# Kernel tuning notes

Hardware: AMD Instinct MI355X
Metric: run time of the kernel (lower is better)

## Reference

```python
import jax, jax.numpy as jnp
import numpy as np

NUM_CODEBOOKS = 32
CODEBOOK_SIZE = 1024
CODE_DIM = 64
BATCH = 4096
INIT_SCALE = 0.1


def setup_inputs() -> dict:
    key = jax.random.key(0)
    k1, k2 = jax.random.split(key)
    z = jax.random.normal(k1, (BATCH, NUM_CODEBOOKS * CODE_DIM), dtype=jnp.float32)
    codebook = jax.random.uniform(
        k2, (NUM_CODEBOOKS, CODEBOOK_SIZE, CODE_DIM),
        minval=-INIT_SCALE, maxval=INIT_SCALE, dtype=jnp.float32)
    return {"z": z, "codebook": codebook}


def reference(z, codebook):
    B = z.shape[0]
    G, K, D = codebook.shape
    z_groups = z.reshape(B, G, D)                                   # [B,G,D]
    # squared euclidean distances: ||z||^2 - 2 z.c + ||c||^2 -> [B,G,K]
    z2 = jnp.sum(z_groups * z_groups, axis=-1, keepdims=True)       # [B,G,1]
    c2 = jnp.sum(codebook * codebook, axis=-1)                      # [G,K]
    zc = jnp.einsum('bgd,gkd->bgk', z_groups, codebook)             # [B,G,K]
    distances = z2 - 2.0 * zc + c2[None, :, :]
    indices = jnp.argmin(distances, axis=-1)                        # [B,G] int
    # gather codebook[g, indices[b,g]] -> [B,G,D]
    z_q_groups = codebook[jnp.arange(G)[None, :], indices]
    commitment_loss = jnp.mean((z_groups - jax.lax.stop_gradient(z_q_groups)) ** 2)
    codebook_loss = jnp.mean((z_q_groups - jax.lax.stop_gradient(z_groups)) ** 2)
    z_st_groups = z_groups + jax.lax.stop_gradient(z_q_groups - z_groups)
    # usage histogram over codebook entries, averaged over (B,G)
    counts = jnp.zeros((K,), dtype=jnp.float32).at[indices.reshape(-1)].add(1.0)
    usage = counts / jnp.float32(B * G)
    entropy = -jnp.sum(usage * jnp.log(usage + 1e-10))
    perplexity = jnp.exp(entropy)
    quantized_flat = z_st_groups.reshape(B, G * D)
    return (quantized_flat, indices, commitment_loss, codebook_loss, entropy, perplexity)
```

## Files before the change

kernel.cpp:

```cpp
#include <hip/hip_runtime.h>
#include <math.h>

#define NG 32
#define NK 1024
#define ND 64
#define NB 4096
#define KSPLIT 4
#define KCHUNK (NK / KSPLIT)


__global__ void vq_init(int* __restrict__ counts, float* __restrict__ losssum) {
    int i = blockIdx.x * blockDim.x + threadIdx.x;
    if (i < NK) counts[i] = 0;
    if (i == 0) *losssum = 0.f;
}

__global__ void vq_c2(const float* __restrict__ cb, float* __restrict__ c2) {
    int i = blockIdx.x * blockDim.x + threadIdx.x;
    if (i >= NG * NK) return;
    const float* c = cb + (size_t)i * ND;
    float s0 = 0.f, s1 = 0.f, s2 = 0.f, s3 = 0.f;
#pragma unroll
    for (int d = 0; d < ND; d += 4) {
        float4 v = *reinterpret_cast<const float4*>(c + d);
        s0 = fmaf(v.x, v.x, s0);
        s1 = fmaf(v.y, v.y, s1);
        s2 = fmaf(v.z, v.z, s2);
        s3 = fmaf(v.w, v.w, s3);
    }
    c2[i] = (s0 + s1) + (s2 + s3);
}

template <int W>
__device__ __forceinline__ float epi_slice(const float* __restrict__ cbest,
                                           float* __restrict__ qrow,
                                           const float (&zv)[ND]) {
    float l0 = 0.f, l1 = 0.f, l2 = 0.f, l3 = 0.f;
#pragma unroll
    for (int i = 0; i < 4; i++) {
        float4 c = reinterpret_cast<const float4*>(cbest)[W * 4 + i];
        float zx = zv[W * 16 + 4 * i + 0], zy = zv[W * 16 + 4 * i + 1];
        float zz = zv[W * 16 + 4 * i + 2], zw = zv[W * 16 + 4 * i + 3];
        float4 st;
        st.x = zx + (c.x - zx);
        st.y = zy + (c.y - zy);
        st.z = zz + (c.z - zz);
        st.w = zw + (c.w - zw);
        reinterpret_cast<float4*>(qrow)[W * 4 + i] = st;
        float dx = zx - c.x, dy = zy - c.y, dz = zz - c.z, dw = zw - c.w;
        l0 = fmaf(dx, dx, l0); l1 = fmaf(dy, dy, l1);
        l2 = fmaf(dz, dz, l2); l3 = fmaf(dw, dw, l3);
    }
    return (l0 + l1) + (l2 + l3);
}

__global__ __launch_bounds__(256) void vq_main(
        const float* __restrict__ z, const float* __restrict__ cb,
        const float* __restrict__ c2, float* __restrict__ qout,
        float* __restrict__ idxout, int* __restrict__ counts,
        float* __restrict__ losssum) {
    const int tid = threadIdx.x;
    const int lane = tid & 63;
    const int wu = __builtin_amdgcn_readfirstlane(tid >> 6);
    const int g = blockIdx.x & (NG - 1);
    const int rowblk = blockIdx.x >> 5;
    const int row = rowblk * 64 + lane;

    const float* zrow = z + (size_t)row * (NG * ND) + (size_t)g * ND;
    float zv[ND];
#pragma unroll
    for (int i = 0; i < ND / 4; i++) {
        float4 v = reinterpret_cast<const float4*>(zrow)[i];
        zv[4 * i + 0] = v.x; zv[4 * i + 1] = v.y;
        zv[4 * i + 2] = v.z; zv[4 * i + 3] = v.w;
    }
    float t0 = 0.f, t1 = 0.f, t2 = 0.f, t3 = 0.f;
#pragma unroll
    for (int d = 0; d < ND; d += 4) {
        t0 = fmaf(zv[d + 0], zv[d + 0], t0);
        t1 = fmaf(zv[d + 1], zv[d + 1], t1);
        t2 = fmaf(zv[d + 2], zv[d + 2], t2);
        t3 = fmaf(zv[d + 3], zv[d + 3], t3);
    }
    const float z2 = (t0 + t1) + (t2 + t3);

    const float* cg = cb + (size_t)g * NK * ND;
    const float* c2g = c2 + (size_t)g * NK;
    const int k0 = wu * KCHUNK;

    float best = 3.402823466e38f;
    int bestk = k0;
#pragma unroll 1
    for (int k = k0; k < k0 + KCHUNK; k++) {
        const float* ck = cg + (size_t)k * ND;
        float a0 = 0.f, a1 = 0.f, a2 = 0.f, a3 = 0.f;
#pragma unroll
        for (int d = 0; d < ND; d += 4) {
            a0 = fmaf(zv[d + 0], ck[d + 0], a0);
            a1 = fmaf(zv[d + 1], ck[d + 1], a1);
            a2 = fmaf(zv[d + 2], ck[d + 2], a2);
            a3 = fmaf(zv[d + 3], ck[d + 3], a3);
        }
        float zc = (a0 + a1) + (a2 + a3);
        float dist = (z2 - 2.0f * zc) + c2g[k];
        if (dist < best) { best = dist; bestk = k; }
    }

    __shared__ float s_best[KSPLIT][64];
    __shared__ int s_bk[KSPLIT][64];
    __shared__ int s_win[64];
    s_best[wu][lane] = best;
    s_bk[wu][lane] = bestk;
    __syncthreads();
    if (wu == 0) {
        float b = s_best[0][lane];
        int bk = s_bk[0][lane];
#pragma unroll
        for (int q = 1; q < KSPLIT; q++) {
            float d = s_best[q][lane];
            int kk = s_bk[q][lane];
            if (d < b) { b = d; bk = kk; }
        }
        s_win[lane] = bk;
        idxout[(size_t)row * NG + g] = (float)bk;
        atomicAdd(&counts[bk], 1);
    }
    __syncthreads();

    const int bk = s_win[lane];
    const float* cbest = cg + (size_t)bk * ND;
    float* qrow = qout + (size_t)row * (NG * ND) + (size_t)g * ND;
    float lsum;
    switch (wu) {
        case 0: lsum = epi_slice<0>(cbest, qrow, zv); break;
        case 1: lsum = epi_slice<1>(cbest, qrow, zv); break;
        case 2: lsum = epi_slice<2>(cbest, qrow, zv); break;
        default: lsum = epi_slice<3>(cbest, qrow, zv); break;
    }
#pragma unroll
    for (int off = 32; off > 0; off >>= 1) lsum += __shfl_down(lsum, off, 64);
    if (lane == 0) atomicAdd(losssum, lsum);
}

__global__ void vq_final(const int* __restrict__ counts,
                         const float* __restrict__ losssum,
                         float* __restrict__ out) {
    __shared__ float red[256];
    int tid = threadIdx.x;
    float e = 0.f;
    for (int k = tid; k < NK; k += 256) {
        float u = (float)counts[k] * (1.0f / 131072.0f);
        e -= u * logf(u + 1e-10f);
    }
    red[tid] = e;
    __syncthreads();
    for (int s = 128; s > 0; s >>= 1) {
        if (tid < s) red[tid] += red[tid + s];
        __syncthreads();
    }
    if (tid == 0) {
        float loss = *losssum * (1.0f / 8388608.0f);
        float ent = red[0];
        out[0] = loss;
        out[1] = loss;
        out[2] = ent;
        out[3] = expf(ent);
    }
}

extern "C" void kernel_launch(void* const* d_in, const int* in_sizes, int n_in,
                              void* d_out, int out_size, void* d_ws, size_t ws_size,
                              hipStream_t stream) {
    const float* z = (const float*)d_in[0];
    const float* cb = (const float*)d_in[1];
    float* out = (float*)d_out;
    float* qout = out;
    float* idxout = out + (size_t)NB * NG * ND;
    float* scal = idxout + (size_t)NB * NG;

    float* c2 = (float*)d_ws;
    int* counts = (int*)(c2 + NG * NK);
    float* losssum = (float*)(counts + NK);

    vq_init<<<(NK + 255) / 256, 256, 0, stream>>>(counts, losssum);
    vq_c2<<<(NG * NK + 255) / 256, 256, 0, stream>>>(cb, c2);
    vq_main<<<(NB / 64) * NG, 256, 0, stream>>>(z, cb, c2, qout, idxout, counts, losssum);
    vq_final<<<1, 256, 0, stream>>>(counts, losssum, scal);
}
```

Before: 502.5 us.

## Software-pipeline codebook loads via VGPR base trick, regroup blocks by codebook, fuse init

The inner distance loop now keeps the next codebook row in registers: it loads row k+1 as float4 quads while doing the FMAs for row k. A zero held in a VGPR is added to the base pointer, which forces per-lane vector loads instead of scalar loads. Block indexing now places the group index in the high bits, so consecutive blocks share the same codebook group for L2 reuse. The init kernel is folded into the c2 kernel, and launch bounds request 3 blocks per CU. The prefetch raises register pressure, and the per-lane loads of identical addresses may cost more than scalar loads.

```diff
diff --git a/kernel.cpp b/kernel.cpp
--- a/kernel.cpp
+++ b/kernel.cpp
@@ -9,14 +9,11 @@
 #define KCHUNK (NK / KSPLIT)
 
 
-__global__ void vq_init(int* __restrict__ counts, float* __restrict__ losssum) {
+__global__ void vq_c2(const float* __restrict__ cb, float* __restrict__ c2,
+                      int* __restrict__ counts, float* __restrict__ losssum) {
     int i = blockIdx.x * blockDim.x + threadIdx.x;
     if (i < NK) counts[i] = 0;
     if (i == 0) *losssum = 0.f;
-}
-
-__global__ void vq_c2(const float* __restrict__ cb, float* __restrict__ c2) {
-    int i = blockIdx.x * blockDim.x + threadIdx.x;
     if (i >= NG * NK) return;
     const float* c = cb + (size_t)i * ND;
     float s0 = 0.f, s1 = 0.f, s2 = 0.f, s3 = 0.f;
@@ -54,7 +51,22 @@
     return (l0 + l1) + (l2 + l3);
 }
 
-__global__ __launch_bounds__(256) void vq_main(
+#define DECLQ(Q) float4 Q##0, Q##1, Q##2, Q##3;
+#define LOADQ(Q, kk, qq) { \
+    const float4* _p = reinterpret_cast<const float4*>( \
+        cbase + ((size_t)(kk) << 8) + ((qq) << 6)); \
+    Q##0 = _p[0]; Q##1 = _p[1]; Q##2 = _p[2]; Q##3 = _p[3]; }
+#define FMAQ(Q, qq) \
+    a0 = fmaf(zv[(qq)*16+ 0], (Q##0).x, a0); a1 = fmaf(zv[(qq)*16+ 1], (Q##0).y, a1); \
+    a2 = fmaf(zv[(qq)*16+ 2], (Q##0).z, a2); a3 = fmaf(zv[(qq)*16+ 3], (Q##0).w, a3); \
+    a0 = fmaf(zv[(qq)*16+ 4], (Q##1).x, a0); a1 = fmaf(zv[(qq)*16+ 5], (Q##1).y, a1); \
+    a2 = fmaf(zv[(qq)*16+ 6], (Q##1).z, a2); a3 = fmaf(zv[(qq)*16+ 7], (Q##1).w, a3); \
+    a0 = fmaf(zv[(qq)*16+ 8], (Q##2).x, a0); a1 = fmaf(zv[(qq)*16+ 9], (Q##2).y, a1); \
+    a2 = fmaf(zv[(qq)*16+10], (Q##2).z, a2); a3 = fmaf(zv[(qq)*16+11], (Q##2).w, a3); \
+    a0 = fmaf(zv[(qq)*16+12], (Q##3).x, a0); a1 = fmaf(zv[(qq)*16+13], (Q##3).y, a1); \
+    a2 = fmaf(zv[(qq)*16+14], (Q##3).z, a2); a3 = fmaf(zv[(qq)*16+15], (Q##3).w, a3);
+
+__global__ __launch_bounds__(256, 3) void vq_main(
         const float* __restrict__ z, const float* __restrict__ cb,
         const float* __restrict__ c2, float* __restrict__ qout,
         float* __restrict__ idxout, int* __restrict__ counts,
@@ -62,8 +74,8 @@
     const int tid = threadIdx.x;
     const int lane = tid & 63;
     const int wu = __builtin_amdgcn_readfirstlane(tid >> 6);
-    const int g = blockIdx.x & (NG - 1);
-    const int rowblk = blockIdx.x >> 5;
+    const int g = blockIdx.x >> 6;
+    const int rowblk = blockIdx.x & 63;
     const int row = rowblk * 64 + lane;
 
     const float* zrow = z + (size_t)row * (NG * ND) + (size_t)g * ND;
@@ -85,25 +97,34 @@
     const float z2 = (t0 + t1) + (t2 + t3);
 
     const float* cg = cb + (size_t)g * NK * ND;
-    const float* c2g = c2 + (size_t)g * NK;
+
+    int vzero;
+    asm volatile("v_mov_b32 %0, 0" : "=v"(vzero));
+    const char* cbase = (const char*)cg + vzero;
+    const char* c2base = (const char*)(c2 + (size_t)g * NK) + vzero;
+
     const int k0 = wu * KCHUNK;
+
+    DECLQ(A) DECLQ(B) DECLQ(C) DECLQ(D)
+    LOADQ(A, k0, 0) LOADQ(B, k0, 1) LOADQ(C, k0, 2) LOADQ(D, k0, 3)
+    float c2cur = *reinterpret_cast<const float*>(c2base + 4 * (size_t)k0);
 
     float best = 3.402823466e38f;
     int bestk = k0;
 #pragma unroll 1
     for (int k = k0; k < k0 + KCHUNK; k++) {
-        const float* ck = cg + (size_t)k * ND;
+        int kn = k + 1;
+        if (kn == k0 + KCHUNK) kn = k0;
+        float c2nxt = *reinterpret_cast<const float*>(c2base + 4 * (size_t)kn);
         float a0 = 0.f, a1 = 0.f, a2 = 0.f, a3 = 0.f;
-#pragma unroll
-        for (int d = 0; d < ND; d += 4) {
-            a0 = fmaf(zv[d + 0], ck[d + 0], a0);
-            a1 = fmaf(zv[d + 1], ck[d + 1], a1);
-            a2 = fmaf(zv[d + 2], ck[d + 2], a2);
-            a3 = fmaf(zv[d + 3], ck[d + 3], a3);
-        }
+        FMAQ(A, 0) LOADQ(A, kn, 0)
+        FMAQ(B, 1) LOADQ(B, kn, 1)
+        FMAQ(C, 2) LOADQ(C, kn, 2)
+        FMAQ(D, 3) LOADQ(D, kn, 3)
         float zc = (a0 + a1) + (a2 + a3);
-        float dist = (z2 - 2.0f * zc) + c2g[k];
+        float dist = (z2 - 2.0f * zc) + c2cur;
         if (dist < best) { best = dist; bestk = k; }
+        c2cur = c2nxt;
     }
 
     __shared__ float s_best[KSPLIT][64];
@@ -182,8 +203,7 @@
     int* counts = (int*)(c2 + NG * NK);
     float* losssum = (float*)(counts + NK);
 
-    vq_init<<<(NK + 255) / 256, 256, 0, stream>>>(counts, losssum);
-    vq_c2<<<(NG * NK + 255) / 256, 256, 0, stream>>>(cb, c2);
-    vq_main<<<(NB / 64) * NG, 256, 0, stream>>>(z, cb, c2, qout, idxout, counts, losssum);
+    vq_c2<<<(NG * NK + 255) / 256, 256, 0, stream>>>(cb, c2, counts, losssum);
+    vq_main<<<NG * (NB / 64), 256, 0, stream>>>(z, cb, c2, qout, idxout, counts, losssum);
     vq_final<<<1, 256, 0, stream>>>(counts, losssum, scal);
 }
```

Result: slower. 1.066 ms (+112.2%).
